# Performance work log

Measured on AMD Instinct MI355X. Metric: run time of the kernel, lower is better.

The kernel has to match this reference:

```python
import jax, jax.numpy as jnp
import numpy as np

EPS = 1e-4
B, C, H, W = 8, 192, 64, 64
HID, DE, N_CLS, CLS_F, E = 256, 64, 8192, 128, 131072
N_IMG = B * H * W


def geolin(x, w):
    # MP_GeoLinear forward: weight-normalized linear, recomputed each call.
    fan = w.shape[1]
    n = jnp.linalg.norm(w, axis=1, keepdims=True)           # per-output-row norm (fp32)
    wn = w / (EPS + n / np.sqrt(fan))                       # normalize() with alpha=1/sqrt(fan)
    return x @ (wn * (1.0 / np.sqrt(fan))).T                # gain/sqrt(fan_in)


def mp_silu(x):
    return jax.nn.silu(x) / 0.596


def mp_cat(a, b, t=0.5):
    Na, Nb = a.shape[1], b.shape[1]
    Cc = np.sqrt((Na + Nb) / ((1 - t) ** 2 + t ** 2))
    return jnp.concatenate([(Cc / np.sqrt(Na) * (1 - t)) * a,
                            (Cc / np.sqrt(Nb) * t) * b], axis=1)


def hetero_conv(x_src, x_dst, src, dst, ea, wl, wr, n_dst):
    # MP_HIPGnnConv: gather -> mp_cat with edge_attr -> mean aggregate -> lin_l,
    # mp_sum with lin_r(x_dst) -> L2 normalize (normalize=True).
    msg = mp_cat(x_src[src], ea)                            # [E, HID+DE]
    s = jax.ops.segment_sum(msg, dst, num_segments=n_dst)
    cnt = jax.ops.segment_sum(jnp.ones((msg.shape[0],), msg.dtype), dst, num_segments=n_dst)
    agg = s / jnp.maximum(cnt, 1.0)[:, None]                # scatter-mean (empty rows -> 0)
    out = (geolin(agg, wl) + geolin(x_dst, wr)) / np.sqrt(2.0)  # mp_sum(t=0.5)
    return out / jnp.maximum(jnp.linalg.norm(out, axis=-1, keepdims=True), 1e-12)


def forward(x, class_x, ea_c2i, ea_i2c,
            w_in_img, w_in_cls,
            wl_c2i_1, wr_c2i_1, wl_i2c_1, wr_i2c_1,
            wl_c2i_2, wr_c2i_2, wl_i2c_2, wr_i2c_2,
            w_out_img, w_out_cls,
            src_c2i, dst_c2i, src_i2c, dst_i2c):
    b, c, h, w = x.shape
    n_img = b * h * w
    n_cls = class_x.shape[0]
    # image pixels become 'image_node' features: [B,C,H,W] -> [B*H*W, C]
    h_img = geolin(jnp.transpose(x, (0, 2, 3, 1)).reshape(-1, c), w_in_img)
    h_cls = geolin(class_x, w_in_cls)
    layers = [(wl_c2i_1, wr_c2i_1, wl_i2c_1, wr_i2c_1),
              (wl_c2i_2, wr_c2i_2, wl_i2c_2, wr_i2c_2)]
    for wl_ci, wr_ci, wl_ic, wr_ic in layers:
        a_img, a_cls = mp_silu(h_img), mp_silu(h_cls)
        h_img = hetero_conv(a_cls, a_img, src_c2i, dst_c2i, ea_c2i, wl_ci, wr_ci, n_img)
        h_cls = hetero_conv(a_img, a_cls, src_i2c, dst_i2c, ea_i2c, wl_ic, wr_ic, n_cls)
    out_img = geolin(h_img, w_out_img).reshape(b, h, w, -1)
    out_img = jnp.transpose(out_img, (0, 3, 1, 2))          # extract_image_nodes
    out_cls = geolin(h_cls, w_out_cls)
    return out_img, out_cls


def setup_inputs() -> dict:
    key = jax.random.key(0)
    ks = jax.random.split(key, 24)
    d = {
        'x': jax.random.normal(ks[0], (B, C, H, W), jnp.float32),
        'class_x': jax.random.normal(ks[1], (N_CLS, CLS_F), jnp.float32),
        'ea_c2i': jax.random.normal(ks[2], (E, DE), jnp.float32),
        'ea_i2c': jax.random.normal(ks[3], (E, DE), jnp.float32),
        'w_in_img': jax.random.normal(ks[4], (HID, C), jnp.float32),
        'w_in_cls': jax.random.normal(ks[5], (HID, CLS_F), jnp.float32),
        'wl_c2i_1': jax.random.normal(ks[6], (HID, HID + DE), jnp.float32),
        'wr_c2i_1': jax.random.normal(ks[7], (HID, HID), jnp.float32),
        'wl_i2c_1': jax.random.normal(ks[8], (HID, HID + DE), jnp.float32),
        'wr_i2c_1': jax.random.normal(ks[9], (HID, HID), jnp.float32),
        'wl_c2i_2': jax.random.normal(ks[10], (HID, HID + DE), jnp.float32),
        'wr_c2i_2': jax.random.normal(ks[11], (HID, HID), jnp.float32),
        'wl_i2c_2': jax.random.normal(ks[12], (HID, HID + DE), jnp.float32),
        'wr_i2c_2': jax.random.normal(ks[13], (HID, HID), jnp.float32),
        'w_out_img': jax.random.normal(ks[14], (HID, HID), jnp.float32),
        'w_out_cls': jax.random.normal(ks[15], (HID, HID), jnp.float32),
        'src_c2i': jax.random.randint(ks[16], (E,), 0, N_CLS, jnp.int32),
        'dst_c2i': jax.random.randint(ks[17], (E,), 0, N_IMG, jnp.int32),
        'src_i2c': jax.random.randint(ks[18], (E,), 0, N_IMG, jnp.int32),
        'dst_i2c': jax.random.randint(ks[19], (E,), 0, N_CLS, jnp.int32),
    }
    return d


def reference(x, class_x, ea_c2i, ea_i2c,
              w_in_img, w_in_cls,
              wl_c2i_1, wr_c2i_1, wl_i2c_1, wr_i2c_1,
              wl_c2i_2, wr_c2i_2, wl_i2c_2, wr_i2c_2,
              w_out_img, w_out_cls,
              src_c2i, dst_c2i, src_i2c, dst_i2c):
    return forward(x, class_x, ea_c2i, ea_i2c,
                   w_in_img, w_in_cls,
                   wl_c2i_1, wr_c2i_1, wl_i2c_1, wr_i2c_1,
                   wl_c2i_2, wr_c2i_2, wl_i2c_2, wr_i2c_2,
                   w_out_img, w_out_cls,
                   src_c2i, dst_c2i, src_i2c, dst_i2c)
```

## Files before the change

### kernel.cpp

```cpp
#include <hip/hip_runtime.h>
#include <cmath>

constexpr int CIN  = 192;
constexpr int HW   = 4096;
constexpr int NIMG = 32768;
constexpr int NCLS = 8192;
constexpr int NE   = 131072;

#define EPSW 1e-4f
#define ALPHA 0.7905694150420949f
#define BETA  1.5811388300841898f
#define SILU_INV 1.6778523489932886f

using bf16x8 = __attribute__((ext_vector_type(8))) __bf16;
using f32x4  = __attribute__((ext_vector_type(4))) float;

__device__ __forceinline__ ushort f2bf(float f) {
  uint u = __float_as_uint(f);
  u = (u + 0x7FFFu + ((u >> 16) & 1u)) >> 16;
  return (ushort)u;
}
__device__ __forceinline__ float bf2f(ushort h) {
  return __uint_as_float(((uint)h) << 16);
}
__device__ __forceinline__ float wave_red_sum(float v) {
  #pragma unroll
  for (int off = 32; off > 0; off >>= 1) v += __shfl_xor(v, off, 64);
  return v;
}
__device__ __forceinline__ int wave_red_sumi(int v) {
  #pragma unroll
  for (int off = 32; off > 0; off >>= 1) v += __shfl_xor(v, off, 64);
  return v;
}
__device__ __forceinline__ uint4 packbf8(float a0, float a1, float a2, float a3,
                                         float a4, float a5, float a6, float a7) {
  uint4 r;
  r.x = (uint)f2bf(a0) | ((uint)f2bf(a1) << 16);
  r.y = (uint)f2bf(a2) | ((uint)f2bf(a3) << 16);
  r.z = (uint)f2bf(a4) | ((uint)f2bf(a5) << 16);
  r.w = (uint)f2bf(a6) | ((uint)f2bf(a7) << 16);
  return r;
}

struct WNA {
  const float* w[12];
  ushort* o[12];
  int F[12];
  int os[12];
  int oo[12];
};
__global__ void wnorm_all_k(WNA a) {
  const int wi = blockIdx.y, row = blockIdx.x, lane = threadIdx.x;
  const int F = a.F[wi];
  const float* wr = a.w[wi] + (size_t)row * F;
  float ss = 0.f;
  for (int f = lane; f < F; f += 64) { float v = wr[f]; ss += v * v; }
  ss = wave_red_sum(ss);
  const float scale = 1.0f / (EPSW * sqrtf((float)F) + sqrtf(ss));
  ushort* o = a.o[wi] + (size_t)row * a.os[wi] + a.oo[wi];
  for (int f = lane; f < F; f += 64) o[f] = f2bf(wr[f] * scale);
}

__global__ void counti_k(const int* __restrict__ d1, const int* __restrict__ d2,
                         int* __restrict__ c1, int* __restrict__ c2) {
  int e = blockIdx.x * 256 + threadIdx.x;
  atomicAdd(&c1[d1[e]], 1);
  atomicAdd(&c2[d2[e]], 1);
}

__global__ __launch_bounds__(256) void scanA_k(const int* __restrict__ cnt,
                                               int* __restrict__ st_img,
                                               int* __restrict__ st_cls,
                                               int* __restrict__ bsum) {
  const int bid = blockIdx.x;
  const bool cls = bid >= 32;
  const int* c = cnt + (cls ? NIMG : 0);
  int* s = cls ? st_cls : st_img;
  const int base = (cls ? bid - 32 : bid) * 1024;
  const int t = threadIdx.x, lane = t & 63, wid = t >> 6;
  int4 v = *(const int4*)(c + base + t * 4);
  const int i0 = v.x, i1 = i0 + v.y, i2 = i1 + v.z, i3 = i2 + v.w;
  int x = i3;
  #pragma unroll
  for (int off = 1; off < 64; off <<= 1) {
    int y = __shfl_up(x, off, 64);
    if (lane >= off) x += y;
  }
  const int pre = x - i3;
  __shared__ int wt[4];
  if (lane == 63) wt[wid] = x;
  __syncthreads();
  int woff = 0;
  #pragma unroll
  for (int i = 0; i < 4; ++i) if (i < wid) woff += wt[i];
  const int b = woff + pre;
  int4 o = { b, b + i0, b + i1, b + i2 };
  *(int4*)(s + base + t * 4) = o;
  if (t == 255) bsum[bid] = woff + x;
}

__global__ __launch_bounds__(256) void scanC_k(const int* __restrict__ bsum,
                                               int* __restrict__ st_img,
                                               int* __restrict__ st_cls) {
  const int bid = blockIdx.x;
  const bool cls = bid >= 32;
  const int seg0 = cls ? 32 : 0;
  const int t = threadIdx.x;
  __shared__ int off_s;
  if (t < 64) {
    int v = (t < bid - seg0) ? bsum[seg0 + t] : 0;
    v = wave_red_sumi(v);
    if (t == 0) off_s = v;
  }
  __syncthreads();
  const int off = off_s;
  int* s = cls ? st_cls : st_img;
  const int base = (cls ? bid - 32 : bid) * 1024;
  int4 v = *(int4*)(s + base + t * 4);
  v.x += off; v.y += off; v.z += off; v.w += off;
  *(int4*)(s + base + t * 4) = v;
  if (bid == 0 && t == 0) { st_img[NIMG] = NE; st_cls[NCLS] = NE; }
}

__global__ void fill2_k(const int* __restrict__ dst1, const int* __restrict__ src1,
                        const int* __restrict__ st1, int* __restrict__ cur1,
                        int2* __restrict__ eix1,
                        const int* __restrict__ dst2, const int* __restrict__ src2,
                        const int* __restrict__ st2, int* __restrict__ cur2,
                        int2* __restrict__ eix2) {
  int e = blockIdx.x * 256 + threadIdx.x;
  int d = dst1[e];
  int p = atomicAdd(&cur1[d], 1);
  eix1[st1[d] + p] = make_int2(e, src1[e]);
  d = dst2[e];
  p = atomicAdd(&cur2[d], 1);
  eix2[st2[d] + p] = make_int2(e, src2[e]);
}

__global__ __launch_bounds__(256) void eam_k(
    const float* __restrict__ ea_ci, const float* __restrict__ ea_ic,
    const int2* __restrict__ eix_ci, const int2* __restrict__ eix_ic,
    const int* __restrict__ st_img, const int* __restrict__ st_cls,
    ushort* __restrict__ eam_img, ushort* __restrict__ eam_cls) {
  const int row  = blockIdx.x * 4 + (threadIdx.x >> 6);
  const int lane = threadIdx.x & 63;
  const float* EA; const int2* eix; const int* st; ushort* out; int r;
  if (row < NIMG) { r = row;        EA = ea_ci; eix = eix_ci; st = st_img;
                    out = eam_img + (size_t)r * 64; }
  else            { r = row - NIMG; EA = ea_ic; eix = eix_ic; st = st_cls;
                    out = eam_cls + (size_t)r * 64; }
  const int s0 = st[r], s1 = st[r + 1];
  float a = 0.f;
  for (int j = s0; j < s1; j += 4) {
    const int i1 = min(j + 1, s1 - 1), i2 = min(j + 2, s1 - 1), i3 = min(j + 3, s1 - 1);
    const int e0 = eix[j].x, e1 = eix[i1].x, e2 = eix[i2].x, e3 = eix[i3].x;
    const float w1 = (j + 1 < s1) ? 1.f : 0.f;
    const float w2 = (j + 2 < s1) ? 1.f : 0.f;
    const float w3 = (j + 3 < s1) ? 1.f : 0.f;
    float v0 = EA[(size_t)e0 * 64 + lane];
    float v1 = EA[(size_t)e1 * 64 + lane];
    float v2 = EA[(size_t)e2 * 64 + lane];
    float v3 = EA[(size_t)e3 * 64 + lane];
    a += v0 + w1 * v1 + w2 * v2 + w3 * v3;
  }
  const float c = BETA / fmaxf((float)(s1 - s0), 1.0f);
  out[lane] = f2bf(a * c);
}

__global__ __launch_bounds__(256) void agg2_k(
    const ushort* __restrict__ Aimg, const ushort* __restrict__ Acls,
    const int2* __restrict__ eix_ci, const int2* __restrict__ eix_ic,
    const int* __restrict__ st_img, const int* __restrict__ st_cls,
    ushort* __restrict__ agg_img, ushort* __restrict__ agg_cls) {
  const int row  = blockIdx.x * 4 + (threadIdx.x >> 6);
  const int lane = threadIdx.x & 63;
  const ushort* Hs; const int2* eix; const int* st; ushort* out; int r;
  if (row < NIMG) { r = row;        Hs = Acls; eix = eix_ci; st = st_img;
                    out = agg_img + (size_t)r * 256; }
  else            { r = row - NIMG; Hs = Aimg; eix = eix_ic; st = st_cls;
                    out = agg_cls + (size_t)r * 256; }
  const int s0 = st[r], s1 = st[r + 1];
  float a0 = 0, a1 = 0, a2 = 0, a3 = 0;
  for (int j = s0; j < s1; j += 4) {
    const int i1 = min(j + 1, s1 - 1), i2 = min(j + 2, s1 - 1), i3 = min(j + 3, s1 - 1);
    const int sA = eix[j].y, sB = eix[i1].y, sC = eix[i2].y, sD = eix[i3].y;
    const float w1 = (j + 1 < s1) ? 1.f : 0.f;
    const float w2 = (j + 2 < s1) ? 1.f : 0.f;
    const float w3 = (j + 3 < s1) ? 1.f : 0.f;
    ushort4 h0 = *(const ushort4*)(Hs + (size_t)sA * 256 + lane * 4);
    ushort4 h1 = *(const ushort4*)(Hs + (size_t)sB * 256 + lane * 4);
    ushort4 h2 = *(const ushort4*)(Hs + (size_t)sC * 256 + lane * 4);
    ushort4 h3 = *(const ushort4*)(Hs + (size_t)sD * 256 + lane * 4);
    a0 += bf2f(h0.x) + w1 * bf2f(h1.x) + w2 * bf2f(h2.x) + w3 * bf2f(h3.x);
    a1 += bf2f(h0.y) + w1 * bf2f(h1.y) + w2 * bf2f(h2.y) + w3 * bf2f(h3.y);
    a2 += bf2f(h0.z) + w1 * bf2f(h1.z) + w2 * bf2f(h2.z) + w3 * bf2f(h3.z);
    a3 += bf2f(h0.w) + w1 * bf2f(h1.w) + w2 * bf2f(h2.w) + w3 * bf2f(h3.w);
  }
  const float c = ALPHA / fmaxf((float)(s1 - s0), 1.0f);
  ushort4 o = { f2bf(a0 * c), f2bf(a1 * c), f2bf(a2 * c), f2bf(a3 * c) };
  *(ushort4*)(out + lane * 4) = o;
}

__device__ __forceinline__ int lds_swz(int row, int kbyte) {
  return ((row << 6) + kbyte) ^ ((row & 7) << 4);
}

__global__ __launch_bounds__(512) void fgemm_k(
    const ushort* __restrict__ AD, const ushort* __restrict__ AG,
    const ushort* __restrict__ EAM, const float* __restrict__ AF,
    const ushort* __restrict__ B, ushort* __restrict__ O,
    int K, int a_mode, int do_norm, int do_silu) {
  __shared__ char ldsb[24576];
  ushort* As = (ushort*)ldsb;
  ushort* Bs = (ushort*)(ldsb + 8192);
  const int t    = threadIdx.x;
  const int row0 = blockIdx.x * 128;
  const int srowA = t >> 2, skA = (t & 3) * 8;
  const int srowB = t >> 1, skB = (t & 1) * 16;
  const int wid = t >> 6, lane = t & 63;
  const int wr = (wid >> 2) * 64, wcq = wid & 3, wc = wcq * 64;
  const int l15 = lane & 15, q = lane >> 4, lk16 = q * 16;
  f32x4 acc[4][4] = {};

  uint4 areg, breg0, breg1;
  auto loadA = [&](int k0) {
    const int row = row0 + srowA;
    if (a_mode == 2) {
      const int kk = k0 + skA;
      const ushort* p = (kk < 256) ? AG + (size_t)row * 256 + kk
                      : (kk < 320) ? EAM + (size_t)row * 64 + (kk - 256)
                                   : AD + (size_t)row * 256 + (kk - 320);
      areg = *(const uint4*)p;
    } else if (a_mode == 3) {
      const float* p = AF + (size_t)row * K + k0 + skA;
      float4 f0 = *(const float4*)p;
      float4 f1 = *(const float4*)(p + 4);
      areg = packbf8(f0.x, f0.y, f0.z, f0.w, f1.x, f1.y, f1.z, f1.w);
    } else {
      const int b = row >> 12, hw = row & 4095;
      const float* p = AF + ((size_t)(b * CIN + k0 + skA)) * HW + hw;
      float f0 = p[0], f1 = p[HW], f2 = p[2 * HW], f3 = p[3 * HW];
      float f4 = p[4 * HW], f5 = p[5 * HW], f6 = p[6 * HW], f7 = p[7 * HW];
      areg = packbf8(f0, f1, f2, f3, f4, f5, f6, f7);
    }
  };
  auto loadB = [&](int k0) {
    const ushort* p = B + (size_t)srowB * K + k0 + skB;
    breg0 = *(const uint4*)p;
    breg1 = *(const uint4*)(p + 8);
  };

  loadA(0); loadB(0);
  for (int k0 = 0; k0 < K; k0 += 32) {
    __syncthreads();
    *(uint4*)((char*)As + lds_swz(srowA, skA * 2)) = areg;
    *(uint4*)((char*)Bs + lds_swz(srowB, skB * 2)) = breg0;
    *(uint4*)((char*)Bs + lds_swz(srowB, skB * 2 + 16)) = breg1;
    __syncthreads();
    if (k0 + 32 < K) { loadA(k0 + 32); loadB(k0 + 32); }
    bf16x8 af[4], bfr[4];
    #pragma unroll
    for (int m = 0; m < 4; ++m)
      af[m] = *(const bf16x8*)((const char*)As + lds_swz(wr + m * 16 + l15, lk16));
    #pragma unroll
    for (int n = 0; n < 4; ++n)
      bfr[n] = *(const bf16x8*)((const char*)Bs + lds_swz(wc + n * 16 + l15, lk16));
    #pragma unroll
    for (int m = 0; m < 4; ++m)
      #pragma unroll
      for (int n = 0; n < 4; ++n)
        acc[m][n] = __builtin_amdgcn_mfma_f32_16x16x32_bf16(af[m], bfr[n], acc[m][n], 0, 0, 0);
  }

  float sc_row[4][4];
  #pragma unroll
  for (int m = 0; m < 4; ++m)
    #pragma unroll
    for (int j = 0; j < 4; ++j) sc_row[m][j] = 1.0f;
  if (do_norm) {
    __syncthreads();
    float* part = (float*)ldsb;
    #pragma unroll
    for (int m = 0; m < 4; ++m)
      #pragma unroll
      for (int j = 0; j < 4; ++j) {
        float ss = 0.f;
        #pragma unroll
        for (int n = 0; n < 4; ++n) { float v = acc[m][n][j]; ss += v * v; }
        ss += __shfl_xor(ss, 1, 64); ss += __shfl_xor(ss, 2, 64);
        ss += __shfl_xor(ss, 4, 64); ss += __shfl_xor(ss, 8, 64);
        if (l15 == 0) part[(wr + m * 16 + q * 4 + j) * 4 + wcq] = ss;
      }
    __syncthreads();
    #pragma unroll
    for (int m = 0; m < 4; ++m)
      #pragma unroll
      for (int j = 0; j < 4; ++j) {
        float4 p4 = *(float4*)&part[(wr + m * 16 + q * 4 + j) * 4];
        sc_row[m][j] = 1.0f / fmaxf(sqrtf(p4.x + p4.y + p4.z + p4.w), 1e-12f);
      }
  }
  #pragma unroll
  for (int m = 0; m < 4; ++m)
    #pragma unroll
    for (int j = 0; j < 4; ++j) {
      const int r = row0 + wr + m * 16 + q * 4 + j;
      #pragma unroll
      for (int n = 0; n < 4; ++n) {
        float v = acc[m][n][j] * sc_row[m][j];
        if (do_silu) v = (v / (1.0f + __expf(-v))) * SILU_INV;
        O[(size_t)r * 256 + wc + n * 16 + l15] = f2bf(v);
      }
    }
}

__global__ __launch_bounds__(256) void mgemm_k(
    const ushort* __restrict__ A, const ushort* __restrict__ B,
    float* __restrict__ C, int K, int ldc, int c_mode) {
  __shared__ ushort As[128 * 32];
  __shared__ ushort Bs[128 * 32];
  const int t    = threadIdx.x;
  const int row0 = blockIdx.x * 128, col0 = blockIdx.y * 128;
  const int srow = t >> 1;
  const int skh  = (t & 1) * 16;
  const int w    = t >> 6, lane = t & 63;
  const int wr   = (w >> 1) * 64, wc = (w & 1) * 64;
  const int l15  = lane & 15, lk16 = (lane >> 4) * 16;
  f32x4 acc[4][4] = {};

  uint4 ar0, ar1, br0, br1;
  auto loadA = [&](int k0) {
    const ushort* p = A + (size_t)(row0 + srow) * K + k0 + skh;
    ar0 = *(const uint4*)(p);
    ar1 = *(const uint4*)(p + 8);
  };
  auto loadB = [&](int k0) {
    const ushort* p = B + (size_t)(col0 + srow) * K + k0 + skh;
    br0 = *(const uint4*)(p);
    br1 = *(const uint4*)(p + 8);
  };

  loadA(0); loadB(0);
  for (int k0 = 0; k0 < K; k0 += 32) {
    __syncthreads();
    *(uint4*)((char*)As + lds_swz(srow, skh * 2))      = ar0;
    *(uint4*)((char*)As + lds_swz(srow, skh * 2 + 16)) = ar1;
    *(uint4*)((char*)Bs + lds_swz(srow, skh * 2))      = br0;
    *(uint4*)((char*)Bs + lds_swz(srow, skh * 2 + 16)) = br1;
    __syncthreads();
    if (k0 + 32 < K) { loadA(k0 + 32); loadB(k0 + 32); }
    bf16x8 af[4], bfr[4];
    #pragma unroll
    for (int m = 0; m < 4; ++m)
      af[m] = *(const bf16x8*)((const char*)As + lds_swz(wr + m * 16 + l15, lk16));
    #pragma unroll
    for (int n = 0; n < 4; ++n)
      bfr[n] = *(const bf16x8*)((const char*)Bs + lds_swz(wc + n * 16 + l15, lk16));
    #pragma unroll
    for (int m = 0; m < 4; ++m)
      #pragma unroll
      for (int n = 0; n < 4; ++n)
        acc[m][n] = __builtin_amdgcn_mfma_f32_16x16x32_bf16(af[m], bfr[n], acc[m][n], 0, 0, 0);
  }

  #pragma unroll
  for (int m = 0; m < 4; ++m) {
    const int rbase = row0 + wr + m * 16 + (lane >> 4) * 4;
    #pragma unroll
    for (int n = 0; n < 4; ++n) {
      const int col = col0 + wc + n * 16 + l15;
      #pragma unroll
      for (int j = 0; j < 4; ++j) {
        const int r = rbase + j;
        if (c_mode == 1)
          C[((size_t)(col >> 12) * 256 + r) * 4096 + (col & 4095)] = acc[m][n][j];
        else
          C[(size_t)r * ldc + col] = acc[m][n][j];
      }
    }
  }
}

extern "C" void kernel_launch(void* const* d_in, const int* in_sizes, int n_in,
                              void* d_out, int out_size, void* d_ws, size_t ws_size,
                              hipStream_t stream) {
  const float* x        = (const float*)d_in[0];
  const float* class_x  = (const float*)d_in[1];
  const float* ea_c2i   = (const float*)d_in[2];
  const float* ea_i2c   = (const float*)d_in[3];
  const int* src_c2i = (const int*)d_in[16];
  const int* dst_c2i = (const int*)d_in[17];
  const int* src_i2c = (const int*)d_in[18];
  const int* dst_i2c = (const int*)d_in[19];

  float* ws = (float*)d_ws;
  size_t off = 0;
  auto alloc = [&](size_t n) { float* p = ws + off; off += (n + 15) & ~(size_t)15; return p; };

  ushort* A_img   = (ushort*)alloc((size_t)NIMG * 128);
  ushort* A_cls   = (ushort*)alloc((size_t)NCLS * 128);
  ushort* H_img   = (ushort*)alloc((size_t)NIMG * 128);
  ushort* H_cls   = (ushort*)alloc((size_t)NCLS * 128);
  ushort* agg_img = (ushort*)alloc((size_t)NIMG * 128);
  ushort* agg_cls = (ushort*)alloc((size_t)NCLS * 128);
  ushort* eam_img = (ushort*)alloc((size_t)NIMG * 32);
  ushort* eam_cls = (ushort*)alloc((size_t)NCLS * 32);
  int* cnt       = (int*)alloc(2 * (NIMG + NCLS));
  int* cur       = cnt + (NIMG + NCLS);
  int* bsum      = (int*)alloc(48);
  int* st_img    = (int*)alloc(NIMG + 1 + NCLS + 1 + 14);
  int* st_cls    = st_img + NIMG + 1;
  int2* eix_c2i  = (int2*)alloc((size_t)NE * 2);
  int2* eix_i2c  = (int2*)alloc((size_t)NE * 2);
  ushort* wn_in_img  = (ushort*)alloc(256 * 96);
  ushort* wn_in_cls  = (ushort*)alloc(256 * 64);
  ushort* wcat0      = (ushort*)alloc(256 * 288);
  ushort* wcat1      = (ushort*)alloc(256 * 288);
  ushort* wcat2      = (ushort*)alloc(256 * 288);
  ushort* wcat3      = (ushort*)alloc(256 * 288);
  ushort* wn_out_img = (ushort*)alloc(256 * 128);
  ushort* wn_out_cls = (ushort*)alloc(256 * 128);

  const dim3 blk(256);

  hipMemsetAsync(cnt, 0, (size_t)2 * (NIMG + NCLS) * sizeof(int), stream);
  counti_k<<<NE / 256, blk, 0, stream>>>(dst_c2i, dst_i2c, cnt, cnt + NIMG);
  scanA_k<<<40, blk, 0, stream>>>(cnt, st_img, st_cls, bsum);
  scanC_k<<<40, blk, 0, stream>>>(bsum, st_img, st_cls);
  fill2_k<<<NE / 256, blk, 0, stream>>>(dst_c2i, src_c2i, st_img, cur, eix_c2i,
                                        dst_i2c, src_i2c, st_cls, cur + NIMG, eix_i2c);
  eam_k<<<(NIMG + NCLS) / 4, blk, 0, stream>>>(ea_c2i, ea_i2c, eix_c2i, eix_i2c,
                                               st_img, st_cls, eam_img, eam_cls);

  WNA wa;
  const float* wsrc[12] = { (const float*)d_in[4], (const float*)d_in[5],
                            (const float*)d_in[6], (const float*)d_in[7],
                            (const float*)d_in[8], (const float*)d_in[9],
                            (const float*)d_in[10], (const float*)d_in[11],
                            (const float*)d_in[12], (const float*)d_in[13],
                            (const float*)d_in[14], (const float*)d_in[15] };
  ushort* wdst[12] = { wn_in_img, wn_in_cls, wcat0, wcat0, wcat1, wcat1,
                       wcat2, wcat2, wcat3, wcat3, wn_out_img, wn_out_cls };
  const int wF[12]  = { 192, 128, 320, 256, 320, 256, 320, 256, 320, 256, 256, 256 };
  const int wOS[12] = { 192, 128, 576, 576, 576, 576, 576, 576, 576, 576, 256, 256 };
  const int wOO[12] = { 0, 0, 0, 320, 0, 320, 0, 320, 0, 320, 0, 0 };
  for (int i = 0; i < 12; ++i) {
    wa.w[i] = wsrc[i]; wa.o[i] = wdst[i]; wa.F[i] = wF[i]; wa.os[i] = wOS[i]; wa.oo[i] = wOO[i];
  }
  wnorm_all_k<<<dim3(256, 12), 64, 0, stream>>>(wa);

  fgemm_k<<<NIMG / 128, 512, 0, stream>>>(nullptr, nullptr, nullptr, x,
                                          wn_in_img, A_img, 192, 1, 0, 1);
  fgemm_k<<<NCLS / 128, 512, 0, stream>>>(nullptr, nullptr, nullptr, class_x,
                                          wn_in_cls, A_cls, 128, 3, 0, 1);

  agg2_k<<<(NIMG + NCLS) / 4, blk, 0, stream>>>(A_img, A_cls, eix_c2i, eix_i2c,
                                                st_img, st_cls, agg_img, agg_cls);
  fgemm_k<<<NIMG / 128, 512, 0, stream>>>(A_img, agg_img, eam_img, nullptr,
                                          wcat0, A_img, 576, 2, 1, 1);
  fgemm_k<<<NCLS / 128, 512, 0, stream>>>(A_cls, agg_cls, eam_cls, nullptr,
                                          wcat1, A_cls, 576, 2, 1, 1);

  agg2_k<<<(NIMG + NCLS) / 4, blk, 0, stream>>>(A_img, A_cls, eix_c2i, eix_i2c,
                                                st_img, st_cls, agg_img, agg_cls);
  fgemm_k<<<NIMG / 128, 512, 0, stream>>>(A_img, agg_img, eam_img, nullptr,
                                          wcat2, H_img, 576, 2, 1, 0);
  fgemm_k<<<NCLS / 128, 512, 0, stream>>>(A_cls, agg_cls, eam_cls, nullptr,
                                          wcat3, H_cls, 576, 2, 1, 0);

  float* out_img = (float*)d_out;
  float* out_cls = (float*)d_out + (size_t)NIMG * 256;
  mgemm_k<<<dim3(2, NIMG / 128), blk, 0, stream>>>(wn_out_img, H_img,
                                                   out_img, 256, 0, 1);
  mgemm_k<<<dim3(NCLS / 128, 2), blk, 0, stream>>>(H_cls, wn_out_cls,
                                                   out_cls, 256, 256, 2);
}
```

Measured before the change: 254.1 us.

## Merge independent kernels into combined launches and fuse edge-attr mean into aggregation

Merges weight normalization with destination counting into one pre-kernel. It also merges each pair of image/class GEMMs and the two output projections into single grid launches that split blocks by index. The separate edge-attribute mean kernel is folded into the first neighbor aggregation pass, which reuses the same edge index loads. This cuts the number of kernel launches and lets small class-side work fill the GPU alongside image work, at the cost of branchier kernels and a runtime flag inside the aggregation loop.

```diff
diff --git a/kernel.cpp b/kernel.cpp
--- a/kernel.cpp
+++ b/kernel.cpp
@@ -50,23 +50,29 @@
   int os[12];
   int oo[12];
 };
-__global__ void wnorm_all_k(WNA a) {
-  const int wi = blockIdx.y, row = blockIdx.x, lane = threadIdx.x;
-  const int F = a.F[wi];
-  const float* wr = a.w[wi] + (size_t)row * F;
-  float ss = 0.f;
-  for (int f = lane; f < F; f += 64) { float v = wr[f]; ss += v * v; }
-  ss = wave_red_sum(ss);
-  const float scale = 1.0f / (EPSW * sqrtf((float)F) + sqrtf(ss));
-  ushort* o = a.o[wi] + (size_t)row * a.os[wi] + a.oo[wi];
-  for (int f = lane; f < F; f += 64) o[f] = f2bf(wr[f] * scale);
-}
-
-__global__ void counti_k(const int* __restrict__ d1, const int* __restrict__ d2,
-                         int* __restrict__ c1, int* __restrict__ c2) {
-  int e = blockIdx.x * 256 + threadIdx.x;
-  atomicAdd(&c1[d1[e]], 1);
-  atomicAdd(&c2[d2[e]], 1);
+__global__ __launch_bounds__(256) void pre_k(WNA a,
+                                             const int* __restrict__ d1,
+                                             const int* __restrict__ d2,
+                                             int* __restrict__ c1,
+                                             int* __restrict__ c2) {
+  const int bx = blockIdx.x, t = threadIdx.x;
+  if (bx < 768) {
+    const int wi = bx >> 6;
+    const int row = ((bx & 63) << 2) + (t >> 6);
+    const int lane = t & 63;
+    const int F = a.F[wi];
+    const float* wr = a.w[wi] + (size_t)row * F;
+    float ss = 0.f;
+    for (int f = lane; f < F; f += 64) { float v = wr[f]; ss += v * v; }
+    ss = wave_red_sum(ss);
+    const float scale = 1.0f / (EPSW * sqrtf((float)F) + sqrtf(ss));
+    ushort* o = a.o[wi] + (size_t)row * a.os[wi] + a.oo[wi];
+    for (int f = lane; f < F; f += 64) o[f] = f2bf(wr[f] * scale);
+  } else {
+    const int e = (bx - 768) * 256 + t;
+    atomicAdd(&c1[d1[e]], 1);
+    atomicAdd(&c2[d2[e]], 1);
+  }
 }
 
 __global__ __launch_bounds__(256) void scanA_k(const int* __restrict__ cnt,
@@ -138,115 +144,98 @@
   eix2[st2[d] + p] = make_int2(e, src2[e]);
 }
 
-__global__ __launch_bounds__(256) void eam_k(
-    const float* __restrict__ ea_ci, const float* __restrict__ ea_ic,
-    const int2* __restrict__ eix_ci, const int2* __restrict__ eix_ic,
-    const int* __restrict__ st_img, const int* __restrict__ st_cls,
-    ushort* __restrict__ eam_img, ushort* __restrict__ eam_cls) {
-  const int row  = blockIdx.x * 4 + (threadIdx.x >> 6);
-  const int lane = threadIdx.x & 63;
-  const float* EA; const int2* eix; const int* st; ushort* out; int r;
-  if (row < NIMG) { r = row;        EA = ea_ci; eix = eix_ci; st = st_img;
-                    out = eam_img + (size_t)r * 64; }
-  else            { r = row - NIMG; EA = ea_ic; eix = eix_ic; st = st_cls;
-                    out = eam_cls + (size_t)r * 64; }
-  const int s0 = st[r], s1 = st[r + 1];
-  float a = 0.f;
-  for (int j = s0; j < s1; j += 4) {
-    const int i1 = min(j + 1, s1 - 1), i2 = min(j + 2, s1 - 1), i3 = min(j + 3, s1 - 1);
-    const int e0 = eix[j].x, e1 = eix[i1].x, e2 = eix[i2].x, e3 = eix[i3].x;
-    const float w1 = (j + 1 < s1) ? 1.f : 0.f;
-    const float w2 = (j + 2 < s1) ? 1.f : 0.f;
-    const float w3 = (j + 3 < s1) ? 1.f : 0.f;
-    float v0 = EA[(size_t)e0 * 64 + lane];
-    float v1 = EA[(size_t)e1 * 64 + lane];
-    float v2 = EA[(size_t)e2 * 64 + lane];
-    float v3 = EA[(size_t)e3 * 64 + lane];
-    a += v0 + w1 * v1 + w2 * v2 + w3 * v3;
-  }
-  const float c = BETA / fmaxf((float)(s1 - s0), 1.0f);
-  out[lane] = f2bf(a * c);
-}
-
 __global__ __launch_bounds__(256) void agg2_k(
     const ushort* __restrict__ Aimg, const ushort* __restrict__ Acls,
     const int2* __restrict__ eix_ci, const int2* __restrict__ eix_ic,
     const int* __restrict__ st_img, const int* __restrict__ st_cls,
-    ushort* __restrict__ agg_img, ushort* __restrict__ agg_cls) {
+    ushort* __restrict__ agg_img, ushort* __restrict__ agg_cls,
+    const float* __restrict__ ea_ci, const float* __restrict__ ea_ic,
+    ushort* __restrict__ eam_img, ushort* __restrict__ eam_cls, int do_eam) {
   const int row  = blockIdx.x * 4 + (threadIdx.x >> 6);
   const int lane = threadIdx.x & 63;
-  const ushort* Hs; const int2* eix; const int* st; ushort* out; int r;
+  const ushort* Hs; const int2* eix; const int* st; ushort* out;
+  const float* EA; ushort* oute; int r;
   if (row < NIMG) { r = row;        Hs = Acls; eix = eix_ci; st = st_img;
-                    out = agg_img + (size_t)r * 256; }
+                    out = agg_img + (size_t)r * 256; EA = ea_ci;
+                    oute = eam_img + (size_t)r * 64; }
   else            { r = row - NIMG; Hs = Aimg; eix = eix_ic; st = st_cls;
-                    out = agg_cls + (size_t)r * 256; }
+                    out = agg_cls + (size_t)r * 256; EA = ea_ic;
+                    oute = eam_cls + (size_t)r * 64; }
   const int s0 = st[r], s1 = st[r + 1];
-  float a0 = 0, a1 = 0, a2 = 0, a3 = 0;
+  float a0 = 0, a1 = 0, a2 = 0, a3 = 0, ae = 0;
   for (int j = s0; j < s1; j += 4) {
     const int i1 = min(j + 1, s1 - 1), i2 = min(j + 2, s1 - 1), i3 = min(j + 3, s1 - 1);
-    const int sA = eix[j].y, sB = eix[i1].y, sC = eix[i2].y, sD = eix[i3].y;
+    const int2 e0 = eix[j], e1 = eix[i1], e2 = eix[i2], e3 = eix[i3];
     const float w1 = (j + 1 < s1) ? 1.f : 0.f;
     const float w2 = (j + 2 < s1) ? 1.f : 0.f;
     const float w3 = (j + 3 < s1) ? 1.f : 0.f;
-    ushort4 h0 = *(const ushort4*)(Hs + (size_t)sA * 256 + lane * 4);
-    ushort4 h1 = *(const ushort4*)(Hs + (size_t)sB * 256 + lane * 4);
-    ushort4 h2 = *(const ushort4*)(Hs + (size_t)sC * 256 + lane * 4);
-    ushort4 h3 = *(const ushort4*)(Hs + (size_t)sD * 256 + lane * 4);
+    ushort4 h0 = *(const ushort4*)(Hs + (size_t)e0.y * 256 + lane * 4);
+    ushort4 h1 = *(const ushort4*)(Hs + (size_t)e1.y * 256 + lane * 4);
+    ushort4 h2 = *(const ushort4*)(Hs + (size_t)e2.y * 256 + lane * 4);
+    ushort4 h3 = *(const ushort4*)(Hs + (size_t)e3.y * 256 + lane * 4);
     a0 += bf2f(h0.x) + w1 * bf2f(h1.x) + w2 * bf2f(h2.x) + w3 * bf2f(h3.x);
     a1 += bf2f(h0.y) + w1 * bf2f(h1.y) + w2 * bf2f(h2.y) + w3 * bf2f(h3.y);
     a2 += bf2f(h0.z) + w1 * bf2f(h1.z) + w2 * bf2f(h2.z) + w3 * bf2f(h3.z);
     a3 += bf2f(h0.w) + w1 * bf2f(h1.w) + w2 * bf2f(h2.w) + w3 * bf2f(h3.w);
-  }
-  const float c = ALPHA / fmaxf((float)(s1 - s0), 1.0f);
+    if (do_eam) {
+      ae += EA[(size_t)e0.x * 64 + lane] + w1 * EA[(size_t)e1.x * 64 + lane]
+          + w2 * EA[(size_t)e2.x * 64 + lane] + w3 * EA[(size_t)e3.x * 64 + lane];
+    }
+  }
+  const float inv = 1.0f / fmaxf((float)(s1 - s0), 1.0f);
+  const float c = ALPHA * inv;
   ushort4 o = { f2bf(a0 * c), f2bf(a1 * c), f2bf(a2 * c), f2bf(a3 * c) };
   *(ushort4*)(out + lane * 4) = o;
+  if (do_eam) oute[lane] = f2bf(ae * BETA * inv);
 }
 
 __device__ __forceinline__ int lds_swz(int row, int kbyte) {
   return ((row << 6) + kbyte) ^ ((row & 7) << 4);
 }
 
-__global__ __launch_bounds__(512) void fgemm_k(
-    const ushort* __restrict__ AD, const ushort* __restrict__ AG,
-    const ushort* __restrict__ EAM, const float* __restrict__ AF,
-    const ushort* __restrict__ B, ushort* __restrict__ O,
-    int K, int a_mode, int do_norm, int do_silu) {
-  __shared__ char ldsb[24576];
+struct FJ {
+  const ushort* AD; const ushort* AG; const ushort* EAM;
+  const float* AF; const ushort* B; ushort* O;
+  int K, a_mode, do_norm, do_silu;
+};
+
+__device__ __forceinline__ void fgemm_body(const FJ J, int bx, char* ldsb) {
   ushort* As = (ushort*)ldsb;
   ushort* Bs = (ushort*)(ldsb + 8192);
   const int t    = threadIdx.x;
-  const int row0 = blockIdx.x * 128;
+  const int row0 = bx * 128;
   const int srowA = t >> 2, skA = (t & 3) * 8;
   const int srowB = t >> 1, skB = (t & 1) * 16;
   const int wid = t >> 6, lane = t & 63;
   const int wr = (wid >> 2) * 64, wcq = wid & 3, wc = wcq * 64;
   const int l15 = lane & 15, q = lane >> 4, lk16 = q * 16;
+  const int K = J.K;
   f32x4 acc[4][4] = {};
 
   uint4 areg, breg0, breg1;
   auto loadA = [&](int k0) {
     const int row = row0 + srowA;
-    if (a_mode == 2) {
+    if (J.a_mode == 2) {
       const int kk = k0 + skA;
-      const ushort* p = (kk < 256) ? AG + (size_t)row * 256 + kk
-                      : (kk < 320) ? EAM + (size_t)row * 64 + (kk - 256)
-                                   : AD + (size_t)row * 256 + (kk - 320);
+      const ushort* p = (kk < 256) ? J.AG + (size_t)row * 256 + kk
+                      : (kk < 320) ? J.EAM + (size_t)row * 64 + (kk - 256)
+                                   : J.AD + (size_t)row * 256 + (kk - 320);
       areg = *(const uint4*)p;
-    } else if (a_mode == 3) {
-      const float* p = AF + (size_t)row * K + k0 + skA;
+    } else if (J.a_mode == 3) {
+      const float* p = J.AF + (size_t)row * K + k0 + skA;
       float4 f0 = *(const float4*)p;
       float4 f1 = *(const float4*)(p + 4);
       areg = packbf8(f0.x, f0.y, f0.z, f0.w, f1.x, f1.y, f1.z, f1.w);
     } else {
       const int b = row >> 12, hw = row & 4095;
-      const float* p = AF + ((size_t)(b * CIN + k0 + skA)) * HW + hw;
+      const float* p = J.AF + ((size_t)(b * CIN + k0 + skA)) * HW + hw;
       float f0 = p[0], f1 = p[HW], f2 = p[2 * HW], f3 = p[3 * HW];
       float f4 = p[4 * HW], f5 = p[5 * HW], f6 = p[6 * HW], f7 = p[7 * HW];
       areg = packbf8(f0, f1, f2, f3, f4, f5, f6, f7);
     }
   };
   auto loadB = [&](int k0) {
-    const ushort* p = B + (size_t)srowB * K + k0 + skB;
+    const ushort* p = J.B + (size_t)srowB * K + k0 + skB;
     breg0 = *(const uint4*)p;
     breg1 = *(const uint4*)(p + 8);
   };
@@ -254,7 +243,7 @@
   loadA(0); loadB(0);
   for (int k0 = 0; k0 < K; k0 += 32) {
     __syncthreads();
-    *(uint4*)((char*)As + lds_swz(srowA, skA * 2)) = areg;
+    *(uint4*)(ldsb + lds_swz(srowA, skA * 2)) = areg;
     *(uint4*)((char*)Bs + lds_swz(srowB, skB * 2)) = breg0;
     *(uint4*)((char*)Bs + lds_swz(srowB, skB * 2 + 16)) = breg1;
     __syncthreads();
@@ -278,7 +267,7 @@
   for (int m = 0; m < 4; ++m)
     #pragma unroll
     for (int j = 0; j < 4; ++j) sc_row[m][j] = 1.0f;
-  if (do_norm) {
+  if (J.do_norm) {
     __syncthreads();
     float* part = (float*)ldsb;
     #pragma unroll
@@ -309,19 +298,26 @@
       #pragma unroll
       for (int n = 0; n < 4; ++n) {
         float v = acc[m][n][j] * sc_row[m][j];
-        if (do_silu) v = (v / (1.0f + __expf(-v))) * SILU_INV;
-        O[(size_t)r * 256 + wc + n * 16 + l15] = f2bf(v);
+        if (J.do_silu) v = (v / (1.0f + __expf(-v))) * SILU_INV;
+        J.O[(size_t)r * 256 + wc + n * 16 + l15] = f2bf(v);
       }
     }
 }
 
-__global__ __launch_bounds__(256) void mgemm_k(
+__global__ __launch_bounds__(512) void fgemm2_k(FJ j0, FJ j1, int n0) {
+  __shared__ char ldsb[24576];
+  const int bx = blockIdx.x;
+  if (bx < n0) fgemm_body(j0, bx, ldsb);
+  else         fgemm_body(j1, bx - n0, ldsb);
+}
+
+__device__ __forceinline__ void mgemm_body(
     const ushort* __restrict__ A, const ushort* __restrict__ B,
-    float* __restrict__ C, int K, int ldc, int c_mode) {
-  __shared__ ushort As[128 * 32];
-  __shared__ ushort Bs[128 * 32];
+    float* __restrict__ C, int K, int ldc, int c_mode,
+    int row0, int col0, char* ldsb) {
+  ushort* As = (ushort*)ldsb;
+  ushort* Bs = (ushort*)(ldsb + 8192);
   const int t    = threadIdx.x;
-  const int row0 = blockIdx.x * 128, col0 = blockIdx.y * 128;
   const int srow = t >> 1;
   const int skh  = (t & 1) * 16;
   const int w    = t >> 6, lane = t & 63;
@@ -379,6 +375,20 @@
           C[(size_t)r * ldc + col] = acc[m][n][j];
       }
     }
+  }
+}
+
+__global__ __launch_bounds__(256) void outproj_k(
+    const ushort* __restrict__ Wimg, const ushort* __restrict__ Himg,
+    float* __restrict__ Oimg, const ushort* __restrict__ Hcls,
+    const ushort* __restrict__ Wcls, float* __restrict__ Ocls) {
+  __shared__ char ldsb[16384];
+  const int bx = blockIdx.x;
+  if (bx < 512)
+    mgemm_body(Wimg, Himg, Oimg, 256, 0, 1, (bx & 1) * 128, (bx >> 1) * 128, ldsb);
+  else {
+    const int b2 = bx - 512;
+    mgemm_body(Hcls, Wcls, Ocls, 256, 256, 2, (b2 >> 1) * 128, (b2 & 1) * 128, ldsb);
   }
 }
 
@@ -425,14 +435,6 @@
   const dim3 blk(256);
 
   hipMemsetAsync(cnt, 0, (size_t)2 * (NIMG + NCLS) * sizeof(int), stream);
-  counti_k<<<NE / 256, blk, 0, stream>>>(dst_c2i, dst_i2c, cnt, cnt + NIMG);
-  scanA_k<<<40, blk, 0, stream>>>(cnt, st_img, st_cls, bsum);
-  scanC_k<<<40, blk, 0, stream>>>(bsum, st_img, st_cls);
-  fill2_k<<<NE / 256, blk, 0, stream>>>(dst_c2i, src_c2i, st_img, cur, eix_c2i,
-                                        dst_i2c, src_i2c, st_cls, cur + NIMG, eix_i2c);
-  eam_k<<<(NIMG + NCLS) / 4, blk, 0, stream>>>(ea_c2i, ea_i2c, eix_c2i, eix_i2c,
-                                               st_img, st_cls, eam_img, eam_cls);
-
   WNA wa;
   const float* wsrc[12] = { (const float*)d_in[4], (const float*)d_in[5],
                             (const float*)d_in[6], (const float*)d_in[7],
@@ -448,31 +450,33 @@
   for (int i = 0; i < 12; ++i) {
     wa.w[i] = wsrc[i]; wa.o[i] = wdst[i]; wa.F[i] = wF[i]; wa.os[i] = wOS[i]; wa.oo[i] = wOO[i];
   }
-  wnorm_all_k<<<dim3(256, 12), 64, 0, stream>>>(wa);
-
-  fgemm_k<<<NIMG / 128, 512, 0, stream>>>(nullptr, nullptr, nullptr, x,
-                                          wn_in_img, A_img, 192, 1, 0, 1);
-  fgemm_k<<<NCLS / 128, 512, 0, stream>>>(nullptr, nullptr, nullptr, class_x,
-                                          wn_in_cls, A_cls, 128, 3, 0, 1);
+  pre_k<<<768 + NE / 256, blk, 0, stream>>>(wa, dst_c2i, dst_i2c, cnt, cnt + NIMG);
+
+  scanA_k<<<40, blk, 0, stream>>>(cnt, st_img, st_cls, bsum);
+  scanC_k<<<40, blk, 0, stream>>>(bsum, st_img, st_cls);
+  fill2_k<<<NE / 256, blk, 0, stream>>>(dst_c2i, src_c2i, st_img, cur, eix_c2i,
+                                        dst_i2c, src_i2c, st_cls, cur + NIMG, eix_i2c);
+
+  FJ jin0 = { nullptr, nullptr, nullptr, x,       wn_in_img, A_img, 192, 1, 0, 1 };
+  FJ jin1 = { nullptr, nullptr, nullptr, class_x, wn_in_cls, A_cls, 128, 3, 0, 1 };
+  fgemm2_k<<<NIMG / 128 + NCLS / 128, 512, 0, stream>>>(jin0, jin1, NIMG / 128);
 
   agg2_k<<<(NIMG + NCLS) / 4, blk, 0, stream>>>(A_img, A_cls, eix_c2i, eix_i2c,
-                                                st_img, st_cls, agg_img, agg_cls);
-  fgemm_k<<<NIMG / 128, 512, 0, stream>>>(A_img, agg_img, eam_img, nullptr,
-                                          wcat0, A_img, 576, 2, 1, 1);
-  fgemm_k<<<NCLS / 128, 512, 0, stream>>>(A_cls, agg_cls, eam_cls, nullptr,
-                                          wcat1, A_cls, 576, 2, 1, 1);
+                                                st_img, st_cls, agg_img, agg_cls,
+                                                ea_c2i, ea_i2c, eam_img, eam_cls, 1);
+  FJ jc10 = { A_img, agg_img, eam_img, nullptr, wcat0, A_img, 576, 2, 1, 1 };
+  FJ jc11 = { A_cls, agg_cls, eam_cls, nullptr, wcat1, A_cls, 576, 2, 1, 1 };
+  fgemm2_k<<<NIMG / 128 + NCLS / 128, 512, 0, stream>>>(jc10, jc11, NIMG / 128);
 
   agg2_k<<<(NIMG + NCLS) / 4, blk, 0, stream>>>(A_img, A_cls, eix_c2i, eix_i2c,
-                                                st_img, st_cls, agg_img, agg_cls);
-  fgemm_k<<<NIMG / 128, 512, 0, stream>>>(A_img, agg_img, eam_img, nullptr,
-                                          wcat2, H_img, 576, 2, 1, 0);
-  fgemm_k<<<NCLS / 128, 512, 0, stream>>>(A_cls, agg_cls, eam_cls, nullptr,
-                                          wcat3, H_cls, 576, 2, 1, 0);
+                                                st_img, st_cls, agg_img, agg_cls,
+                                                nullptr, nullptr, nullptr, nullptr, 0);
+  FJ jc20 = { A_img, agg_img, eam_img, nullptr, wcat2, H_img, 576, 2, 1, 0 };
+  FJ jc21 = { A_cls, agg_cls, eam_cls, nullptr, wcat3, H_cls, 576, 2, 1, 0 };
+  fgemm2_k<<<NIMG / 128 + NCLS / 128, 512, 0, stream>>>(jc20, jc21, NIMG / 128);
 
   float* out_img = (float*)d_out;
   float* out_cls = (float*)d_out + (size_t)NIMG * 256;
-  mgemm_k<<<dim3(2, NIMG / 128), blk, 0, stream>>>(wn_out_img, H_img,
-                                                   out_img, 256, 0, 1);
-  mgemm_k<<<dim3(NCLS / 128, 2), blk, 0, stream>>>(H_cls, wn_out_cls,
-                                                   out_cls, 256, 256, 2);
-}
+  outproj_k<<<640, blk, 0, stream>>>(wn_out_img, H_img, out_img,
+                                     H_cls, wn_out_cls, out_cls);
+}
```

Measured after the change: 227.0 us. -10.7%, faster.
